# Kernel tuning notes

Measured on AMD Instinct MI355X. Metric: run time of the kernel, lower is better.

The kernel has to match this reference:

```python
import jax, jax.numpy as jnp
import numpy as np

N, D, K = 8192, 2048, 256
# amnesic weights at train iteration 0: _i = 2 < n1 = 20 -> l = 0
W1 = 0.5  # (_i - 1 - l) / _i
W2 = 0.5  # (1 + l) / _i


def setup_inputs() -> dict:
    key = jax.random.key(0)
    k1, k2 = jax.random.split(key)
    x = jax.random.normal(k1, (N, D), dtype=jnp.float32)
    V0 = 0.1 * jax.random.normal(k2, (D, K), dtype=jnp.float32)  # init eigen vectors
    return {"x": x, "V0": V0}


def reference(x, V0):
    # x: [N, D] input batch; V0: [D, K] unnormalized eigenvector estimates (_v)
    d0 = jnp.linalg.norm(V0, axis=0)  # per-column norms, as in init_eigen_vectors setter

    def step(r, inp):
        v, d = inp  # v: [D] current unnormalized component, d: scalar norm
        # CCIPCA update: v' = w1*v + w2 * r^T (r v) / d
        u = W1 * v + (W2 / d) * (r.T @ (r @ v))
        dn = jnp.linalg.norm(u)
        vn = u / dn
        # deflate residual: r <- r - (r vn) vn^T
        r = r - jnp.outer(r @ vn, vn)
        return r, vn

    _, vns = jax.lax.scan(step, x, (V0.T, d0))  # vns: [K, D] normalized components
    # project original input on updated components: x.mm(self.v)
    return x @ vns.T  # [N, K]
```

## Files before the change

### kernel.cpp

```cpp
#include <hip/hip_runtime.h>
#include <math.h>

#define NN 8192
#define DD 2048
#define KK 256
#define NB 256
#define RPB 8
#define NGRP 16
#define GSZ 16

__device__ __forceinline__ float blockReduceSum(float val, float* sdata) {
    for (int off = 32; off > 0; off >>= 1)
        val += __shfl_down(val, off, 64);
    int wid = threadIdx.x >> 6;
    int lane = threadIdx.x & 63;
    __syncthreads();
    if (lane == 0) sdata[wid] = val;
    __syncthreads();
    return sdata[0] + sdata[1] + sdata[2] + sdata[3];
}

__device__ __forceinline__ float agload(const float* p) {
    return __hip_atomic_load(p, __ATOMIC_RELAXED, __HIP_MEMORY_SCOPE_AGENT);
}
__device__ __forceinline__ void agstore(float* p, float v) {
    __hip_atomic_store(p, v, __ATOMIC_RELAXED, __HIP_MEMORY_SCOPE_AGENT);
}

__device__ __forceinline__ void gbar2(unsigned* bar, int b, unsigned* gen_local) {
    __syncthreads();
    if (threadIdx.x == 0) {
        unsigned g0 = *gen_local;
        int grp = b >> 4;
        unsigned* gcnt = bar + (size_t)grp * 64;
        unsigned* ggen = bar + 1024 + (size_t)grp * 64;
        unsigned* rcnt = bar + 2048;
        unsigned* rgen = bar + 2112;
        unsigned prev = __hip_atomic_fetch_add(gcnt, 1u, __ATOMIC_RELAXED, __HIP_MEMORY_SCOPE_AGENT);
        if (prev == GSZ - 1u) {
            unsigned prevr = __hip_atomic_fetch_add(rcnt, 1u, __ATOMIC_RELAXED, __HIP_MEMORY_SCOPE_AGENT);
            if (prevr == NGRP - 1u) {
                __hip_atomic_store(rcnt, 0u, __ATOMIC_RELAXED, __HIP_MEMORY_SCOPE_AGENT);
                asm volatile("s_waitcnt vmcnt(0)" ::: "memory");
                __hip_atomic_store(rgen, g0 + 1u, __ATOMIC_RELAXED, __HIP_MEMORY_SCOPE_AGENT);
            } else {
                while (__hip_atomic_load(rgen, __ATOMIC_RELAXED, __HIP_MEMORY_SCOPE_AGENT) == g0)
                    __builtin_amdgcn_s_sleep(1);
            }
            __hip_atomic_store(gcnt, 0u, __ATOMIC_RELAXED, __HIP_MEMORY_SCOPE_AGENT);
            asm volatile("s_waitcnt vmcnt(0)" ::: "memory");
            __hip_atomic_store(ggen, g0 + 1u, __ATOMIC_RELAXED, __HIP_MEMORY_SCOPE_AGENT);
        } else {
            while (__hip_atomic_load(ggen, __ATOMIC_RELAXED, __HIP_MEMORY_SCOPE_AGENT) == g0)
                __builtin_amdgcn_s_sleep(1);
        }
    }
    *gen_local += 1u;
    __syncthreads();
}

__global__ void ktranspose(const float* __restrict__ V0, float* __restrict__ V0T) {
    __shared__ float tile[32][33];
    int bx = blockIdx.x;
    int by = blockIdx.y;
    int tx = threadIdx.x % 32;
    int ty = threadIdx.x / 32;
    for (int r = ty; r < 32; r += 8)
        tile[r][tx] = V0[(size_t)(bx * 32 + r) * KK + by * 32 + tx];
    __syncthreads();
    for (int r = ty; r < 32; r += 8)
        V0T[(size_t)(by * 32 + r) * DD + bx * 32 + tx] = tile[tx][r];
}

__global__ void kd0(const float* __restrict__ V0T, float* __restrict__ d0) {
    __shared__ float sdata[4];
    int k = blockIdx.x;
    float acc = 0.f;
    for (int j = threadIdx.x; j < DD; j += 256) {
        float v = V0T[(size_t)k * DD + j];
        acc += v * v;
    }
    float s = blockReduceSum(acc, sdata);
    if (threadIdx.x == 0) d0[k] = sqrtf(s);
}

__global__ void ksyrk(const float* __restrict__ x, float* __restrict__ G) {
    __shared__ float As[32][68];
    __shared__ float Bs[32][68];
    int t = blockIdx.x;
    int bj = (int)((sqrtf(8.0f * (float)t + 1.0f) - 1.0f) * 0.5f);
    while ((bj + 1) * (bj + 2) / 2 <= t) ++bj;
    while (bj * (bj + 1) / 2 > t) --bj;
    int bi = t - bj * (bj + 1) / 2;
    int a0 = bi * 64, b0 = bj * 64;
    int tid = threadIdx.x;
    int al = tid % 64;
    int nl0 = tid / 64;
    int tr = tid / 16, tc = tid % 16;
    float acc[4][4] = {};
    for (int n0 = 0; n0 < NN; n0 += 32) {
        for (int pass = 0; pass < 8; ++pass) {
            int nl = nl0 + pass * 4;
            As[nl][al] = x[(size_t)(n0 + nl) * DD + a0 + al];
            Bs[nl][al] = x[(size_t)(n0 + nl) * DD + b0 + al];
        }
        __syncthreads();
        for (int kk2 = 0; kk2 < 32; ++kk2) {
            float4 a4 = *(const float4*)&As[kk2][tr * 4];
            float4 b4 = *(const float4*)&Bs[kk2][tc * 4];
            float a[4] = {a4.x, a4.y, a4.z, a4.w};
            float b[4] = {b4.x, b4.y, b4.z, b4.w};
            for (int i = 0; i < 4; ++i)
                for (int j = 0; j < 4; ++j)
                    acc[i][j] += a[i] * b[j];
        }
        __syncthreads();
    }
    for (int i = 0; i < 4; ++i) {
        float4 o = make_float4(acc[i][0], acc[i][1], acc[i][2], acc[i][3]);
        *(float4*)&G[(size_t)(a0 + tr * 4 + i) * DD + b0 + tc * 4] = o;
    }
    if (bi != bj) {
        for (int i = 0; i < 4; ++i)
            for (int j = 0; j < 4; ++j)
                G[(size_t)(b0 + tc * 4 + j) * DD + a0 + tr * 4 + i] = acc[i][j];
    }
}

__global__ void kmatvecG(const float* __restrict__ G, const float* __restrict__ v,
                         float* __restrict__ s) {
    __shared__ float vs[DD];
    int tid = threadIdx.x;
    for (int t2 = 0; t2 < 8; ++t2) vs[tid + t2 * 256] = v[tid + t2 * 256];
    __syncthreads();
    int wave = tid >> 6, lane = tid & 63;
    int row = blockIdx.x * 4 + wave;
    const float* Gr = G + (size_t)row * DD;
    float a = 0.f;
    for (int c = 0; c < 8; ++c) {
        int idx = lane * 4 + c * 256;
        float4 gq = *(const float4*)(Gr + idx);
        float4 vq = *(const float4*)(vs + idx);
        a += gq.x * vq.x + gq.y * vq.y + gq.z * vq.z + gq.w * vq.w;
    }
    for (int off = 32; off > 0; off >>= 1) a += __shfl_down(a, off, 64);
    if (lane == 0) s[row] = a;
}

__global__ void kstep1(const float* __restrict__ G, const float* __restrict__ V0T,
                       const float* __restrict__ d0, const float* __restrict__ s,
                       float* __restrict__ g, float* __restrict__ Vn, int k) {
    __shared__ float u[DD];
    __shared__ float sdata[4];
    __shared__ float sinv;
    int tid = threadIdx.x;
    const float* v = V0T + (size_t)k * DD;
    float cf = 0.5f / d0[k];
    float acc = 0.f;
    for (int t2 = 0; t2 < 8; ++t2) {
        int j = tid + t2 * 256;
        float uj = 0.5f * v[j] + cf * s[j];
        u[j] = uj;
        acc += uj * uj;
    }
    float n2 = blockReduceSum(acc, sdata);
    if (tid == 0) sinv = 1.0f / sqrtf(n2);
    __syncthreads();
    float inv = sinv;
    if (blockIdx.x == 0) {
        for (int t2 = 0; t2 < 8; ++t2) {
            int j = tid + t2 * 256;
            Vn[(size_t)k * DD + j] = u[j] * inv;
        }
    }
    int wave = tid >> 6, lane = tid & 63;
    int row = blockIdx.x * 4 + wave;
    const float* Gr = G + (size_t)row * DD;
    float a = 0.f;
    for (int c = 0; c < 8; ++c) {
        int idx = lane * 4 + c * 256;
        float4 gq = *(const float4*)(Gr + idx);
        float4 uq = *(const float4*)(u + idx);
        a += gq.x * uq.x + gq.y * uq.y + gq.z * uq.z + gq.w * uq.w;
    }
    for (int off = 32; off > 0; off >>= 1) a += __shfl_down(a, off, 64);
    if (lane == 0) g[row] = a * inv;
}

__global__ void kstep2(float* __restrict__ G, const float* __restrict__ V0T,
                       const float* __restrict__ Vn, const float* __restrict__ g,
                       float* __restrict__ s_next, int k, int knext) {
    __shared__ float vn_s[DD];
    __shared__ float h_s[DD];
    __shared__ float w_s[DD];
    __shared__ float sdata[4];
    int tid = threadIdx.x;
    float acc = 0.f;
    for (int t2 = 0; t2 < 8; ++t2) {
        int j = tid + t2 * 256;
        float vnj = Vn[(size_t)k * DD + j];
        float gj = g[j];
        vn_s[j] = vnj;
        h_s[j] = gj;
        w_s[j] = V0T[(size_t)knext * DD + j];
        acc += vnj * gj;
    }
    float c = blockReduceSum(acc, sdata);
    for (int t2 = 0; t2 < 8; ++t2) {
        int j = tid + t2 * 256;
        h_s[j] -= c * vn_s[j];
    }
    __syncthreads();
    int wave = tid >> 6, lane = tid & 63;
    int row = blockIdx.x * 4 + wave;
    float vni = vn_s[row], gi = g[row];
    float* Gr = G + (size_t)row * DD;
    float a = 0.f;
    for (int cc = 0; cc < 8; ++cc) {
        int idx = lane * 4 + cc * 256;
        float4 Gq = *(float4*)(Gr + idx);
        float4 hq = *(const float4*)(h_s + idx);
        float4 vq = *(const float4*)(vn_s + idx);
        float4 wq = *(const float4*)(w_s + idx);
        Gq.x = Gq.x - vni * hq.x - gi * vq.x;
        Gq.y = Gq.y - vni * hq.y - gi * vq.y;
        Gq.z = Gq.z - vni * hq.z - gi * vq.z;
        Gq.w = Gq.w - vni * hq.w - gi * vq.w;
        a += Gq.x * wq.x + Gq.y * wq.y + Gq.z * wq.z + Gq.w * wq.w;
        *(float4*)(Gr + idx) = Gq;
    }
    for (int off = 32; off > 0; off >>= 1) a += __shfl_down(a, off, 64);
    if (lane == 0) s_next[row] = a;
}

__global__ void __launch_bounds__(1024, 4) kloop2(
    float* __restrict__ G, const float* __restrict__ V0T,
    const float* __restrict__ d0, float* __restrict__ Vn,
    float* __restrict__ gbuf, float* __restrict__ wbuf,
    unsigned* bar) {
    __shared__ float vbuf[2][DD];
    __shared__ float gs[DD];
    __shared__ float vx[DD];
    __shared__ float redA[16], redB[16], redC[16];
    __shared__ float partg[16], partw[16];
    const int tid = threadIdx.x;
    const int b = blockIdx.x;
    const int wave = tid >> 6, lane = tid & 63;
    const int rowi = wave >> 1;
    const int half = wave & 1;
    const int row = b * RPB + rowi;
    float* Gr = G + (size_t)row * DD;
    unsigned gen = 0;

    vbuf[0][tid] = 0.f;
    vbuf[0][tid + 1024] = 0.f;
    vx[tid] = V0T[tid];
    vx[tid + 1024] = V0T[tid + 1024];
    __syncthreads();
    {
        float aw = 0.f;
        for (int c = 0; c < 4; ++c) {
            int idx = half * 1024 + lane * 4 + c * 256;
            float4 g4 = *(const float4*)(Gr + idx);
            float4 x4 = *(const float4*)(vx + idx);
            aw += g4.x * x4.x + g4.y * x4.y + g4.z * x4.z + g4.w * x4.w;
        }
        for (int off = 32; off > 0; off >>= 1) aw += __shfl_down(aw, off, 64);
        if (lane == 0) partw[wave] = aw;
    }
    __syncthreads();
    if (tid < RPB)
        agstore(&wbuf[b * RPB + tid], partw[2 * tid] + partw[2 * tid + 1]);
    gbar2(bar, b, &gen);

    for (int k = 0; k < KK; ++k) {
        const int p = k & 1;
        const float* vnp = vbuf[p];
        float* vnew = vbuf[p ^ 1];
        const float* gsrc = gbuf + (size_t)p * DD;
        const float* wsrc = wbuf + (size_t)p * DD;
        float* gdst = gbuf + (size_t)(p ^ 1) * DD;
        float* wdst = wbuf + (size_t)(p ^ 1) * DD;
        const float* vk = V0T + (size_t)k * DD;

        float vk0 = vk[tid], vk1 = vk[tid + 1024];
        float g0 = agload(&gsrc[tid]), g1 = agload(&gsrc[tid + 1024]);
        gs[tid] = g0;
        gs[tid + 1024] = g1;
        float vp0 = vnp[tid], vp1 = vnp[tid + 1024];
        float pc = vp0 * g0 + vp1 * g1;
        float pgv = g0 * vk0 + g1 * vk1;
        float pbv = vp0 * vk0 + vp1 * vk1;
        for (int off = 32; off > 0; off >>= 1) {
            pc += __shfl_down(pc, off, 64);
            pgv += __shfl_down(pgv, off, 64);
            pbv += __shfl_down(pbv, off, 64);
        }
        __syncthreads();
        if (lane == 0) { redA[wave] = pc; redB[wave] = pgv; redC[wave] = pbv; }
        __syncthreads();
        float c_s = 0.f, gv = 0.f, bv = 0.f;
        for (int i = 0; i < 16; ++i) { c_s += redA[i]; gv += redB[i]; bv += redC[i]; }
        float alpha = gv - c_s * bv;
        float beta = bv;

        float cf = 0.5f / d0[k];
        float w0 = agload(&wsrc[tid]), w1 = agload(&wsrc[tid + 1024]);
        float u0 = 0.5f * vk0 + cf * (w0 - alpha * vp0 - beta * g0);
        float u1 = 0.5f * vk1 + cf * (w1 - alpha * vp1 - beta * g1);
        float pn = u0 * u0 + u1 * u1;
        for (int off = 32; off > 0; off >>= 1) pn += __shfl_down(pn, off, 64);
        __syncthreads();
        if (lane == 0) redA[wave] = pn;
        __syncthreads();
        float n2 = 0.f;
        for (int i = 0; i < 16; ++i) n2 += redA[i];
        float inv = 1.0f / sqrtf(n2);

        if (b == 0) {
            Vn[(size_t)k * DD + tid] = u0 * inv;
            Vn[(size_t)k * DD + tid + 1024] = u1 * inv;
        }
        if (k == KK - 1) break;

        vnew[tid] = u0 * inv;
        vnew[tid + 1024] = u1 * inv;
        const float* vkn = V0T + (size_t)(k + 1) * DD;
        vx[tid] = vkn[tid];
        vx[tid + 1024] = vkn[tid + 1024];
        __syncthreads();

        {
            float a_r = vnp[row];
            float g_r = gs[row];
            float b_r = g_r - c_s * a_r;
            float ag = 0.f, aw = 0.f;
            for (int c = 0; c < 4; ++c) {
                int idx = half * 1024 + lane * 4 + c * 256;
                float4 G4 = *(float4*)(Gr + idx);
                float4 gq = *(const float4*)(gs + idx);
                float4 vq = *(const float4*)(vnp + idx);
                float4 nq = *(const float4*)(vnew + idx);
                float4 xq = *(const float4*)(vx + idx);
                G4.x -= a_r * gq.x + b_r * vq.x;
                G4.y -= a_r * gq.y + b_r * vq.y;
                G4.z -= a_r * gq.z + b_r * vq.z;
                G4.w -= a_r * gq.w + b_r * vq.w;
                ag += G4.x * nq.x + G4.y * nq.y + G4.z * nq.z + G4.w * nq.w;
                aw += G4.x * xq.x + G4.y * xq.y + G4.z * xq.z + G4.w * xq.w;
                *(float4*)(Gr + idx) = G4;
            }
            for (int off = 32; off > 0; off >>= 1) {
                ag += __shfl_down(ag, off, 64);
                aw += __shfl_down(aw, off, 64);
            }
            if (lane == 0) { partg[wave] = ag; partw[wave] = aw; }
        }
        __syncthreads();
        if (tid < RPB) {
            int r = b * RPB + tid;
            agstore(&gdst[r], partg[2 * tid] + partg[2 * tid + 1]);
            agstore(&wdst[r], partw[2 * tid] + partw[2 * tid + 1]);
        }
        gbar2(bar, b, &gen);
    }
}

__global__ void kout(const float* __restrict__ x, const float* __restrict__ Vn,
                     float* __restrict__ out) {
    __shared__ float As[32][68];
    __shared__ float Bs[32][68];
    int i0 = blockIdx.x * 64;
    int k0 = blockIdx.y * 64;
    int tid = threadIdx.x;
    int tr = tid / 16;
    int tc = tid % 16;
    float acc[4][4] = {};
    for (int j0 = 0; j0 < DD; j0 += 32) {
        int c = tid % 32;
        int r0 = tid / 32;
        for (int pass = 0; pass < 8; ++pass) {
            int rr = r0 + pass * 8;
            As[c][rr] = x[(size_t)(i0 + rr) * DD + j0 + c];
            Bs[c][rr] = Vn[(size_t)(k0 + rr) * DD + j0 + c];
        }
        __syncthreads();
        for (int kk = 0; kk < 32; ++kk) {
            float4 a4 = *(const float4*)&As[kk][tr * 4];
            float4 b4 = *(const float4*)&Bs[kk][tc * 4];
            float a[4] = {a4.x, a4.y, a4.z, a4.w};
            float b[4] = {b4.x, b4.y, b4.z, b4.w};
            for (int ar = 0; ar < 4; ++ar)
                for (int bc = 0; bc < 4; ++bc)
                    acc[ar][bc] += a[ar] * b[bc];
        }
        __syncthreads();
    }
    for (int ar = 0; ar < 4; ++ar) {
        float4 o = make_float4(acc[ar][0], acc[ar][1], acc[ar][2], acc[ar][3]);
        *(float4*)&out[(size_t)(i0 + tr * 4 + ar) * KK + k0 + tc * 4] = o;
    }
}

extern "C" void kernel_launch(void* const* d_in, const int* in_sizes, int n_in,
                              void* d_out, int out_size, void* d_ws, size_t ws_size,
                              hipStream_t stream) {
    const float* x  = (const float*)d_in[0];
    const float* V0 = (const float*)d_in[1];
    float* out = (float*)d_out;

    float* G    = (float*)d_ws;
    float* V0T  = G + (size_t)DD * DD;
    float* Vn   = V0T + (size_t)KK * DD;
    float* gbuf = Vn + (size_t)KK * DD;
    float* wbuf = gbuf + 2 * DD;
    float* d0   = wbuf + 2 * DD;
    unsigned* bar = (unsigned*)(d0 + KK);

    ktranspose<<<dim3(DD / 32, KK / 32), 256, 0, stream>>>(V0, V0T);
    kd0<<<KK, 256, 0, stream>>>(V0T, d0);
    ksyrk<<<528, 256, 0, stream>>>(x, G);

    hipMemsetAsync(bar, 0, 2176 * sizeof(unsigned), stream);
    hipMemsetAsync(gbuf, 0, DD * sizeof(float), stream);

    void* kargs[] = {(void*)&G, (void*)&V0T, (void*)&d0, (void*)&Vn,
                     (void*)&gbuf, (void*)&wbuf, (void*)&bar};
    hipError_t cerr = hipLaunchCooperativeKernel(kloop2, dim3(NB), dim3(1024),
                                                 kargs, 0, stream);
    if (cerr != hipSuccess) {
        float* g = gbuf;
        float* sbuf = wbuf;
        kmatvecG<<<512, 256, 0, stream>>>(G, V0T, sbuf);
        for (int k = 0; k < KK; ++k) {
            float* s_cur = sbuf + (k & 1) * DD;
            float* s_nxt = sbuf + ((k + 1) & 1) * DD;
            kstep1<<<512, 256, 0, stream>>>(G, V0T, d0, s_cur, g, Vn, k);
            if (k < KK - 1)
                kstep2<<<512, 256, 0, stream>>>(G, V0T, Vn, g, s_nxt, k, k + 1);
        }
    }

    kout<<<dim3(NN / 64, KK / 64), 256, 0, stream>>>(x, Vn, out);
}
```

Baseline: 2.872 ms.

## Defer Gram-matrix deflation updates into windowed blocked flushes

The persistent cooperative kernel used to rewrite the whole 2048x2048 Gram matrix G after every component. It now keeps a window of up to 8 pending rank-2 deflations, held as Vn and a new gwinG buffer, and applies them lazily. The matvec results are corrected with small dot-product reductions, and G is read once per step but written only at flush time. This cuts the global read-modify-write traffic on G, at the cost of extra reductions, syncs and global loads of the window vectors on each step.

```diff
diff --git a/kernel.cpp b/kernel.cpp
--- a/kernel.cpp
+++ b/kernel.cpp
@@ -8,6 +8,7 @@
 #define RPB 8
 #define NGRP 16
 #define GSZ 16
+#define TW 8
 
 __device__ __forceinline__ float blockReduceSum(float val, float* sdata) {
     for (int off = 32; off > 0; off >>= 1)
@@ -233,34 +234,41 @@
     if (lane == 0) s_next[row] = a;
 }
 
-__global__ void __launch_bounds__(1024, 4) kloop2(
+__global__ void __launch_bounds__(1024, 4) kloop3(
     float* __restrict__ G, const float* __restrict__ V0T,
-    const float* __restrict__ d0, float* __restrict__ Vn,
+    const float* __restrict__ d0v, float* __restrict__ Vn,
+    float* __restrict__ gwinG,
     float* __restrict__ gbuf, float* __restrict__ wbuf,
     unsigned* bar) {
-    __shared__ float vbuf[2][DD];
-    __shared__ float gs[DD];
+    __shared__ float vnew[DD];
     __shared__ float vx[DD];
-    __shared__ float redA[16], redB[16], redC[16];
+    __shared__ float stv[DD];
+    __shared__ float stg[DD];
+    __shared__ float redC[18][16];
+    __shared__ float redS[18];
+    __shared__ float redN[16];
     __shared__ float partg[16], partw[16];
+    __shared__ float cwin[TW];
+
     const int tid = threadIdx.x;
     const int b = blockIdx.x;
     const int wave = tid >> 6, lane = tid & 63;
     const int rowi = wave >> 1;
     const int half = wave & 1;
     const int row = b * RPB + rowi;
+    const int d0i = tid, d1i = tid + 1024;
+    const int ib = half * 1024 + lane * 4;
     float* Gr = G + (size_t)row * DD;
     unsigned gen = 0;
 
-    vbuf[0][tid] = 0.f;
-    vbuf[0][tid + 1024] = 0.f;
-    vx[tid] = V0T[tid];
-    vx[tid + 1024] = V0T[tid + 1024];
+    vx[d0i] = V0T[d0i];
+    vx[d1i] = V0T[d1i];
     __syncthreads();
     {
         float aw = 0.f;
+        #pragma unroll
         for (int c = 0; c < 4; ++c) {
-            int idx = half * 1024 + lane * 4 + c * 256;
+            int idx = ib + c * 256;
             float4 g4 = *(const float4*)(Gr + idx);
             float4 x4 = *(const float4*)(vx + idx);
             aw += g4.x * x4.x + g4.y * x4.y + g4.z * x4.z + g4.w * x4.w;
@@ -273,88 +281,227 @@
         agstore(&wbuf[b * RPB + tid], partw[2 * tid] + partw[2 * tid + 1]);
     gbar2(bar, b, &gen);
 
+    int base = 0;
     for (int k = 0; k < KK; ++k) {
         const int p = k & 1;
-        const float* vnp = vbuf[p];
-        float* vnew = vbuf[p ^ 1];
         const float* gsrc = gbuf + (size_t)p * DD;
         const float* wsrc = wbuf + (size_t)p * DD;
         float* gdst = gbuf + (size_t)(p ^ 1) * DD;
         float* wdst = wbuf + (size_t)(p ^ 1) * DD;
         const float* vk = V0T + (size_t)k * DD;
 
-        float vk0 = vk[tid], vk1 = vk[tid + 1024];
-        float g0 = agload(&gsrc[tid]), g1 = agload(&gsrc[tid + 1024]);
-        gs[tid] = g0;
-        gs[tid + 1024] = g1;
-        float vp0 = vnp[tid], vp1 = vnp[tid + 1024];
-        float pc = vp0 * g0 + vp1 * g1;
-        float pgv = g0 * vk0 + g1 * vk1;
-        float pbv = vp0 * vk0 + vp1 * vk1;
-        for (int off = 32; off > 0; off >>= 1) {
-            pc += __shfl_down(pc, off, 64);
-            pgv += __shfl_down(pgv, off, 64);
-            pbv += __shfl_down(pbv, off, 64);
-        }
-        __syncthreads();
-        if (lane == 0) { redA[wave] = pc; redB[wave] = pgv; redC[wave] = pbv; }
-        __syncthreads();
-        float c_s = 0.f, gv = 0.f, bv = 0.f;
-        for (int i = 0; i < 16; ++i) { c_s += redA[i]; gv += redB[i]; bv += redC[i]; }
-        float alpha = gv - c_s * bv;
-        float beta = bv;
-
-        float cf = 0.5f / d0[k];
-        float w0 = agload(&wsrc[tid]), w1 = agload(&wsrc[tid + 1024]);
-        float u0 = 0.5f * vk0 + cf * (w0 - alpha * vp0 - beta * g0);
-        float u1 = 0.5f * vk1 + cf * (w1 - alpha * vp1 - beta * g1);
+        float gh0 = agload(&gsrc[d0i]), gh1 = agload(&gsrc[d1i]);
+        float wh0 = agload(&wsrc[d0i]), wh1 = agload(&wsrc[d1i]);
+        float vk0 = vk[d0i], vk1 = vk[d1i];
+
+        const int pend = k - 1;
+        const int mc1 = (k > 0) ? (pend - base) : 0;
+        const int mc2 = (k > 0) ? (k - base) : 0;
+
+        float wv0[7], wv1[7], wg0[7], wg1[7];
+        #pragma unroll
+        for (int jj = 0; jj < 7; ++jj) {
+            if (jj < mc1) {
+                const float* vj = Vn + (size_t)(base + jj) * DD;
+                const float* gj = gwinG + (size_t)(base + jj) * DD;
+                wv0[jj] = vj[d0i]; wv1[jj] = vj[d1i];
+                wg0[jj] = gj[d0i]; wg1[jj] = gj[d1i];
+            }
+        }
+
+        float gc0 = gh0, gc1 = gh1;
+        float vp0 = 0.f, vp1 = 0.f;
+        if (k > 0) { vp0 = vnew[d0i]; vp1 = vnew[d1i]; }
+        if (mc1 > 0) {
+            #pragma unroll
+            for (int jj = 0; jj < 7; ++jj) {
+                if (jj < mc1) {
+                    float pa = wg0[jj] * vp0 + wg1[jj] * vp1;
+                    float pb = wv0[jj] * vp0 + wv1[jj] * vp1;
+                    for (int off = 32; off > 0; off >>= 1) {
+                        pa += __shfl_down(pa, off, 64);
+                        pb += __shfl_down(pb, off, 64);
+                    }
+                    if (lane == 0) { redC[2 * jj][wave] = pa; redC[2 * jj + 1][wave] = pb; }
+                }
+            }
+            __syncthreads();
+            if (wave == 0 && lane < 2 * mc1) {
+                float s = 0.f;
+                for (int w = 0; w < 16; ++w) s += redC[lane][w];
+                redS[lane] = s;
+            }
+            __syncthreads();
+            #pragma unroll
+            for (int jj = 0; jj < 7; ++jj) {
+                if (jj < mc1) {
+                    float A_ = redS[2 * jj], B_ = redS[2 * jj + 1];
+                    float cj = cwin[jj];
+                    float hA = A_ - cj * B_;
+                    gc0 -= wv0[jj] * hA + wg0[jj] * B_;
+                    gc1 -= wv1[jj] * hA + wg1[jj] * B_;
+                }
+            }
+        }
+
+        float c_s = 0.f;
+        float s0 = wh0, s1 = wh1;
+        if (k > 0) {
+            float pc = vp0 * gc0 + vp1 * gc1;
+            for (int off = 32; off > 0; off >>= 1) pc += __shfl_down(pc, off, 64);
+            if (lane == 0) redC[0][wave] = pc;
+            #pragma unroll
+            for (int jj = 0; jj < 7; ++jj) {
+                if (jj < mc1) {
+                    float pP = wg0[jj] * vk0 + wg1[jj] * vk1;
+                    float pQ = wv0[jj] * vk0 + wv1[jj] * vk1;
+                    for (int off = 32; off > 0; off >>= 1) {
+                        pP += __shfl_down(pP, off, 64);
+                        pQ += __shfl_down(pQ, off, 64);
+                    }
+                    if (lane == 0) { redC[1 + 2 * jj][wave] = pP; redC[2 + 2 * jj][wave] = pQ; }
+                }
+            }
+            {
+                float pP = gc0 * vk0 + gc1 * vk1;
+                float pQ = vp0 * vk0 + vp1 * vk1;
+                for (int off = 32; off > 0; off >>= 1) {
+                    pP += __shfl_down(pP, off, 64);
+                    pQ += __shfl_down(pQ, off, 64);
+                }
+                if (lane == 0) { redC[1 + 2 * mc1][wave] = pP; redC[2 + 2 * mc1][wave] = pQ; }
+            }
+            __syncthreads();
+            int nv = 1 + 2 * mc2;
+            if (wave == 0 && lane < nv) {
+                float s = 0.f;
+                for (int w = 0; w < 16; ++w) s += redC[lane][w];
+                redS[lane] = s;
+            }
+            __syncthreads();
+            c_s = redS[0];
+            if (tid == 0) cwin[pend & (TW - 1)] = c_s;
+            #pragma unroll
+            for (int jj = 0; jj < 7; ++jj) {
+                if (jj < mc1) {
+                    float P_ = redS[1 + 2 * jj], Q_ = redS[2 + 2 * jj];
+                    float cj = cwin[jj];
+                    float hP = P_ - cj * Q_;
+                    s0 -= wv0[jj] * hP + wg0[jj] * Q_;
+                    s1 -= wv1[jj] * hP + wg1[jj] * Q_;
+                }
+            }
+            {
+                float P_ = redS[1 + 2 * mc1], Q_ = redS[2 + 2 * mc1];
+                float hP = P_ - c_s * Q_;
+                s0 -= vp0 * hP + gc0 * Q_;
+                s1 -= vp1 * hP + gc1 * Q_;
+            }
+        }
+
+        float cf = 0.5f / d0v[k];
+        float u0 = 0.5f * vk0 + cf * s0;
+        float u1 = 0.5f * vk1 + cf * s1;
         float pn = u0 * u0 + u1 * u1;
         for (int off = 32; off > 0; off >>= 1) pn += __shfl_down(pn, off, 64);
-        __syncthreads();
-        if (lane == 0) redA[wave] = pn;
-        __syncthreads();
+        if (lane == 0) redN[wave] = pn;
+        __syncthreads();
+
+        const bool flush = (k < KK - 1) && (mc2 == TW);
+        if (flush) {
+            stv[d0i] = vp0; stv[d1i] = vp1;
+            stg[d0i] = gc0; stg[d1i] = gc1;
+        }
         float n2 = 0.f;
-        for (int i = 0; i < 16; ++i) n2 += redA[i];
+        #pragma unroll
+        for (int w = 0; w < 16; ++w) n2 += redN[w];
         float inv = 1.0f / sqrtf(n2);
-
+        float o0 = u0 * inv, o1 = u1 * inv;
+        vnew[d0i] = o0;
+        vnew[d1i] = o1;
         if (b == 0) {
-            Vn[(size_t)k * DD + tid] = u0 * inv;
-            Vn[(size_t)k * DD + tid + 1024] = u1 * inv;
+            agstore(&Vn[(size_t)k * DD + d0i], o0);
+            agstore(&Vn[(size_t)k * DD + d1i], o1);
+            if (k > 0) {
+                agstore(&gwinG[(size_t)pend * DD + d0i], gc0);
+                agstore(&gwinG[(size_t)pend * DD + d1i], gc1);
+            }
         }
         if (k == KK - 1) break;
-
-        vnew[tid] = u0 * inv;
-        vnew[tid + 1024] = u1 * inv;
-        const float* vkn = V0T + (size_t)(k + 1) * DD;
-        vx[tid] = vkn[tid];
-        vx[tid + 1024] = vkn[tid + 1024];
-        __syncthreads();
+        vx[d0i] = V0T[(size_t)(k + 1) * DD + d0i];
+        vx[d1i] = V0T[(size_t)(k + 1) * DD + d1i];
+        __syncthreads();
+
+        float4 Gq0 = *(float4*)(Gr + ib);
+        float4 Gq1 = *(float4*)(Gr + ib + 256);
+        float4 Gq2 = *(float4*)(Gr + ib + 512);
+        float4 Gq3 = *(float4*)(Gr + ib + 768);
+
+        if (flush) {
+            {
+                float av = stv[row];
+                float agr = stg[row];
+                float bv = agr - c_s * av;
+                #pragma unroll
+                for (int c = 0; c < 4; ++c) {
+                    int idx = ib + c * 256;
+                    float4 sg = *(const float4*)(stg + idx);
+                    float4 sv = *(const float4*)(stv + idx);
+                    float4* Gq = (c == 0) ? &Gq0 : (c == 1) ? &Gq1 : (c == 2) ? &Gq2 : &Gq3;
+                    Gq->x -= av * sg.x + bv * sv.x;
+                    Gq->y -= av * sg.y + bv * sv.y;
+                    Gq->z -= av * sg.z + bv * sv.z;
+                    Gq->w -= av * sg.w + bv * sv.w;
+                }
+            }
+            #pragma unroll
+            for (int jj = 0; jj < TW - 1; ++jj) {
+                __syncthreads();
+                const float* vj = Vn + (size_t)(base + jj) * DD;
+                const float* gj = gwinG + (size_t)(base + jj) * DD;
+                stv[d0i] = vj[d0i]; stv[d1i] = vj[d1i];
+                stg[d0i] = gj[d0i]; stg[d1i] = gj[d1i];
+                __syncthreads();
+                float av = stv[row];
+                float agr = stg[row];
+                float bv = agr - cwin[jj] * av;
+                #pragma unroll
+                for (int c = 0; c < 4; ++c) {
+                    int idx = ib + c * 256;
+                    float4 sg = *(const float4*)(stg + idx);
+                    float4 sv = *(const float4*)(stv + idx);
+                    float4* Gq = (c == 0) ? &Gq0 : (c == 1) ? &Gq1 : (c == 2) ? &Gq2 : &Gq3;
+                    Gq->x -= av * sg.x + bv * sv.x;
+                    Gq->y -= av * sg.y + bv * sv.y;
+                    Gq->z -= av * sg.z + bv * sv.z;
+                    Gq->w -= av * sg.w + bv * sv.w;
+                }
+            }
+            base = k;
+        }
 
         {
-            float a_r = vnp[row];
-            float g_r = gs[row];
-            float b_r = g_r - c_s * a_r;
-            float ag = 0.f, aw = 0.f;
+            float agd = 0.f, awd = 0.f;
+            #pragma unroll
             for (int c = 0; c < 4; ++c) {
-                int idx = half * 1024 + lane * 4 + c * 256;
-                float4 G4 = *(float4*)(Gr + idx);
-                float4 gq = *(const float4*)(gs + idx);
-                float4 vq = *(const float4*)(vnp + idx);
+                int idx = ib + c * 256;
                 float4 nq = *(const float4*)(vnew + idx);
                 float4 xq = *(const float4*)(vx + idx);
-                G4.x -= a_r * gq.x + b_r * vq.x;
-                G4.y -= a_r * gq.y + b_r * vq.y;
-                G4.z -= a_r * gq.z + b_r * vq.z;
-                G4.w -= a_r * gq.w + b_r * vq.w;
-                ag += G4.x * nq.x + G4.y * nq.y + G4.z * nq.z + G4.w * nq.w;
-                aw += G4.x * xq.x + G4.y * xq.y + G4.z * xq.z + G4.w * xq.w;
-                *(float4*)(Gr + idx) = G4;
+                float4 Gq = (c == 0) ? Gq0 : (c == 1) ? Gq1 : (c == 2) ? Gq2 : Gq3;
+                agd += Gq.x * nq.x + Gq.y * nq.y + Gq.z * nq.z + Gq.w * nq.w;
+                awd += Gq.x * xq.x + Gq.y * xq.y + Gq.z * xq.z + Gq.w * xq.w;
+            }
+            if (flush) {
+                *(float4*)(Gr + ib) = Gq0;
+                *(float4*)(Gr + ib + 256) = Gq1;
+                *(float4*)(Gr + ib + 512) = Gq2;
+                *(float4*)(Gr + ib + 768) = Gq3;
             }
             for (int off = 32; off > 0; off >>= 1) {
-                ag += __shfl_down(ag, off, 64);
-                aw += __shfl_down(aw, off, 64);
-            }
-            if (lane == 0) { partg[wave] = ag; partw[wave] = aw; }
+                agd += __shfl_down(agd, off, 64);
+                awd += __shfl_down(awd, off, 64);
+            }
+            if (lane == 0) { partg[wave] = agd; partw[wave] = awd; }
         }
         __syncthreads();
         if (tid < RPB) {
@@ -409,12 +556,13 @@
     const float* V0 = (const float*)d_in[1];
     float* out = (float*)d_out;
 
-    float* G    = (float*)d_ws;
-    float* V0T  = G + (size_t)DD * DD;
-    float* Vn   = V0T + (size_t)KK * DD;
-    float* gbuf = Vn + (size_t)KK * DD;
-    float* wbuf = gbuf + 2 * DD;
-    float* d0   = wbuf + 2 * DD;
+    float* G     = (float*)d_ws;
+    float* V0T   = G + (size_t)DD * DD;
+    float* Vn    = V0T + (size_t)KK * DD;
+    float* gwinG = Vn + (size_t)KK * DD;
+    float* gbuf  = gwinG + (size_t)KK * DD;
+    float* wbuf  = gbuf + 2 * DD;
+    float* d0    = wbuf + 2 * DD;
     unsigned* bar = (unsigned*)(d0 + KK);
 
     ktranspose<<<dim3(DD / 32, KK / 32), 256, 0, stream>>>(V0, V0T);
@@ -422,11 +570,10 @@
     ksyrk<<<528, 256, 0, stream>>>(x, G);
 
     hipMemsetAsync(bar, 0, 2176 * sizeof(unsigned), stream);
-    hipMemsetAsync(gbuf, 0, DD * sizeof(float), stream);
 
     void* kargs[] = {(void*)&G, (void*)&V0T, (void*)&d0, (void*)&Vn,
-                     (void*)&gbuf, (void*)&wbuf, (void*)&bar};
-    hipError_t cerr = hipLaunchCooperativeKernel(kloop2, dim3(NB), dim3(1024),
+                     (void*)&gwinG, (void*)&gbuf, (void*)&wbuf, (void*)&bar};
+    hipError_t cerr = hipLaunchCooperativeKernel(kloop3, dim3(NB), dim3(1024),
                                                  kargs, 0, stream);
     if (cerr != hipSuccess) {
         float* g = gbuf;
```

Result: slower. 4.039 ms (+40.6%).

## Keep G rows in registers and precompute step scalars via global atomics

Applied to the files above, without the earlier changes.

Each block now keeps its slice of the deflated Gram matrix in registers across all 256 iterations instead of reloading and storing it from global memory every step. The per-step block reductions (dot products and the norm of u) are replaced by eight scalar accumulators. All blocks add into these with atomics during the previous step, and the norm is reconstructed algebraically, which removes several __syncthreads/reduction rounds per iteration. Vn output is written distributed across blocks. The risk is higher register pressure and possible cancellation error in the expanded norm formula.

```diff
diff --git a/kernel.cpp b/kernel.cpp
--- a/kernel.cpp
+++ b/kernel.cpp
@@ -233,44 +233,61 @@
     if (lane == 0) s_next[row] = a;
 }
 
-__global__ void __launch_bounds__(1024, 4) kloop2(
+__global__ void __launch_bounds__(1024, 4) kloop4(
     float* __restrict__ G, const float* __restrict__ V0T,
-    const float* __restrict__ d0, float* __restrict__ Vn,
+    const float* __restrict__ d0v, float* __restrict__ Vn,
     float* __restrict__ gbuf, float* __restrict__ wbuf,
-    unsigned* bar) {
+    float* __restrict__ acc, unsigned* bar) {
     __shared__ float vbuf[2][DD];
     __shared__ float gs[DD];
     __shared__ float vx[DD];
-    __shared__ float redA[16], redB[16], redC[16];
     __shared__ float partg[16], partw[16];
+
     const int tid = threadIdx.x;
     const int b = blockIdx.x;
     const int wave = tid >> 6, lane = tid & 63;
     const int rowi = wave >> 1;
     const int half = wave & 1;
     const int row = b * RPB + rowi;
-    float* Gr = G + (size_t)row * DD;
+    const int d0i = tid, d1i = tid + 1024;
+    const int ib = half * 1024 + lane * 4;
+    const float* Gr = G + (size_t)row * DD;
     unsigned gen = 0;
 
-    vbuf[0][tid] = 0.f;
-    vbuf[0][tid + 1024] = 0.f;
-    vx[tid] = V0T[tid];
-    vx[tid + 1024] = V0T[tid + 1024];
+    float4 Gq[4];
+    #pragma unroll
+    for (int c = 0; c < 4; ++c) Gq[c] = *(const float4*)(Gr + ib + c * 256);
+
+    vbuf[0][d0i] = 0.f;
+    vbuf[0][d1i] = 0.f;
+    vx[d0i] = V0T[d0i];
+    vx[d1i] = V0T[d1i];
     __syncthreads();
     {
         float aw = 0.f;
+        #pragma unroll
         for (int c = 0; c < 4; ++c) {
-            int idx = half * 1024 + lane * 4 + c * 256;
-            float4 g4 = *(const float4*)(Gr + idx);
-            float4 x4 = *(const float4*)(vx + idx);
-            aw += g4.x * x4.x + g4.y * x4.y + g4.z * x4.z + g4.w * x4.w;
+            float4 xq = *(const float4*)(vx + ib + c * 256);
+            aw += Gq[c].x * xq.x + Gq[c].y * xq.y + Gq[c].z * xq.z + Gq[c].w * xq.w;
         }
         for (int off = 32; off > 0; off >>= 1) aw += __shfl_down(aw, off, 64);
         if (lane == 0) partw[wave] = aw;
     }
     __syncthreads();
-    if (tid < RPB)
-        agstore(&wbuf[b * RPB + tid], partw[2 * tid] + partw[2 * tid + 1]);
+    if (tid < RPB) {
+        int rg = b * RPB + tid;
+        agstore(&wbuf[rg], partw[2 * tid] + partw[2 * tid + 1]);
+    }
+    if (tid == 0) {
+        float a4 = 0.f, a7 = 0.f;
+        for (int r = 0; r < RPB; ++r) {
+            float wr = partw[2 * r] + partw[2 * r + 1];
+            a4 += wr * wr;
+            a7 += wr * vx[b * RPB + r];
+        }
+        atomicAdd(&acc[3], a4);
+        atomicAdd(&acc[6], a7);
+    }
     gbar2(bar, b, &gen);
 
     for (int k = 0; k < KK; ++k) {
@@ -282,73 +299,62 @@
         float* gdst = gbuf + (size_t)(p ^ 1) * DD;
         float* wdst = wbuf + (size_t)(p ^ 1) * DD;
         const float* vk = V0T + (size_t)k * DD;
-
-        float vk0 = vk[tid], vk1 = vk[tid + 1024];
-        float g0 = agload(&gsrc[tid]), g1 = agload(&gsrc[tid + 1024]);
-        gs[tid] = g0;
-        gs[tid + 1024] = g1;
-        float vp0 = vnp[tid], vp1 = vnp[tid + 1024];
-        float pc = vp0 * g0 + vp1 * g1;
-        float pgv = g0 * vk0 + g1 * vk1;
-        float pbv = vp0 * vk0 + vp1 * vk1;
-        for (int off = 32; off > 0; off >>= 1) {
-            pc += __shfl_down(pc, off, 64);
-            pgv += __shfl_down(pgv, off, 64);
-            pbv += __shfl_down(pbv, off, 64);
-        }
-        __syncthreads();
-        if (lane == 0) { redA[wave] = pc; redB[wave] = pgv; redC[wave] = pbv; }
-        __syncthreads();
-        float c_s = 0.f, gv = 0.f, bv = 0.f;
-        for (int i = 0; i < 16; ++i) { c_s += redA[i]; gv += redB[i]; bv += redC[i]; }
-        float alpha = gv - c_s * bv;
-        float beta = bv;
-
-        float cf = 0.5f / d0[k];
-        float w0 = agload(&wsrc[tid]), w1 = agload(&wsrc[tid + 1024]);
+        const float* as = acc + (size_t)k * 8;
+
+        float A1 = agload(&as[0]), A2 = agload(&as[1]), A3 = agload(&as[2]);
+        float A4 = agload(&as[3]), A5 = agload(&as[4]), A6 = agload(&as[5]);
+        float A7 = agload(&as[6]), A8 = agload(&as[7]);
+        float d0k = d0v[k];
+        float cf = 0.5f / d0k;
+        float c_s = A1;
+        float alpha = A2 - A1 * A3;
+        float beta = A3;
+        float ss = A4 + alpha * alpha + beta * beta * A8
+                 - 2.f * alpha * A6 - 2.f * beta * A5 + 2.f * alpha * beta * A1;
+        float vks = A7 - alpha * A3 - beta * A2;
+        float n2 = 0.25f * d0k * d0k + cf * vks + cf * cf * ss;
+        float inv = 1.0f / sqrtf(n2);
+
+        float g0 = agload(&gsrc[d0i]), g1 = agload(&gsrc[d1i]);
+        float w0 = agload(&wsrc[d0i]), w1 = agload(&wsrc[d1i]);
+        float vk0 = vk[d0i], vk1 = vk[d1i];
+        float vp0 = vnp[d0i], vp1 = vnp[d1i];
+        gs[d0i] = g0;
+        gs[d1i] = g1;
         float u0 = 0.5f * vk0 + cf * (w0 - alpha * vp0 - beta * g0);
         float u1 = 0.5f * vk1 + cf * (w1 - alpha * vp1 - beta * g1);
-        float pn = u0 * u0 + u1 * u1;
-        for (int off = 32; off > 0; off >>= 1) pn += __shfl_down(pn, off, 64);
-        __syncthreads();
-        if (lane == 0) redA[wave] = pn;
-        __syncthreads();
-        float n2 = 0.f;
-        for (int i = 0; i < 16; ++i) n2 += redA[i];
-        float inv = 1.0f / sqrtf(n2);
-
-        if (b == 0) {
-            Vn[(size_t)k * DD + tid] = u0 * inv;
-            Vn[(size_t)k * DD + tid + 1024] = u1 * inv;
+        vnew[d0i] = u0 * inv;
+        vnew[d1i] = u1 * inv;
+        if (k < KK - 1) {
+            vx[d0i] = V0T[(size_t)(k + 1) * DD + d0i];
+            vx[d1i] = V0T[(size_t)(k + 1) * DD + d1i];
+        }
+        __syncthreads();
+
+        if (tid < RPB) {
+            int rg = b * RPB + tid;
+            agstore(&Vn[(size_t)k * DD + rg], vnew[rg]);
         }
         if (k == KK - 1) break;
-
-        vnew[tid] = u0 * inv;
-        vnew[tid + 1024] = u1 * inv;
-        const float* vkn = V0T + (size_t)(k + 1) * DD;
-        vx[tid] = vkn[tid];
-        vx[tid + 1024] = vkn[tid + 1024];
-        __syncthreads();
 
         {
             float a_r = vnp[row];
             float g_r = gs[row];
             float b_r = g_r - c_s * a_r;
             float ag = 0.f, aw = 0.f;
+            #pragma unroll
             for (int c = 0; c < 4; ++c) {
-                int idx = half * 1024 + lane * 4 + c * 256;
-                float4 G4 = *(float4*)(Gr + idx);
+                int idx = ib + c * 256;
                 float4 gq = *(const float4*)(gs + idx);
                 float4 vq = *(const float4*)(vnp + idx);
                 float4 nq = *(const float4*)(vnew + idx);
                 float4 xq = *(const float4*)(vx + idx);
-                G4.x -= a_r * gq.x + b_r * vq.x;
-                G4.y -= a_r * gq.y + b_r * vq.y;
-                G4.z -= a_r * gq.z + b_r * vq.z;
-                G4.w -= a_r * gq.w + b_r * vq.w;
-                ag += G4.x * nq.x + G4.y * nq.y + G4.z * nq.z + G4.w * nq.w;
-                aw += G4.x * xq.x + G4.y * xq.y + G4.z * xq.z + G4.w * xq.w;
-                *(float4*)(Gr + idx) = G4;
+                Gq[c].x -= a_r * gq.x + b_r * vq.x;
+                Gq[c].y -= a_r * gq.y + b_r * vq.y;
+                Gq[c].z -= a_r * gq.z + b_r * vq.z;
+                Gq[c].w -= a_r * gq.w + b_r * vq.w;
+                ag += Gq[c].x * nq.x + Gq[c].y * nq.y + Gq[c].z * nq.z + Gq[c].w * nq.w;
+                aw += Gq[c].x * xq.x + Gq[c].y * xq.y + Gq[c].z * xq.z + Gq[c].w * xq.w;
             }
             for (int off = 32; off > 0; off >>= 1) {
                 ag += __shfl_down(ag, off, 64);
@@ -358,9 +364,32 @@
         }
         __syncthreads();
         if (tid < RPB) {
-            int r = b * RPB + tid;
-            agstore(&gdst[r], partg[2 * tid] + partg[2 * tid + 1]);
-            agstore(&wdst[r], partw[2 * tid] + partw[2 * tid + 1]);
+            int rg = b * RPB + tid;
+            agstore(&gdst[rg], partg[2 * tid] + partg[2 * tid + 1]);
+            agstore(&wdst[rg], partw[2 * tid] + partw[2 * tid + 1]);
+        }
+        if (tid < 8) {
+            float sacc = 0.f;
+            for (int r = 0; r < RPB; ++r) {
+                int rg = b * RPB + r;
+                float gr = partg[2 * r] + partg[2 * r + 1];
+                float wr = partw[2 * r] + partw[2 * r + 1];
+                float vnr = vnew[rg];
+                float vxr = vx[rg];
+                float t;
+                switch (tid) {
+                    case 0: t = vnr * gr; break;
+                    case 1: t = gr * vxr; break;
+                    case 2: t = vnr * vxr; break;
+                    case 3: t = wr * wr; break;
+                    case 4: t = wr * gr; break;
+                    case 5: t = wr * vnr; break;
+                    case 6: t = wr * vxr; break;
+                    default: t = gr * gr; break;
+                }
+                sacc += t;
+            }
+            atomicAdd(&acc[(size_t)(k + 1) * 8 + tid], sacc);
         }
         gbar2(bar, b, &gen);
     }
@@ -415,7 +444,8 @@
     float* gbuf = Vn + (size_t)KK * DD;
     float* wbuf = gbuf + 2 * DD;
     float* d0   = wbuf + 2 * DD;
-    unsigned* bar = (unsigned*)(d0 + KK);
+    float* acc  = d0 + KK;
+    unsigned* bar = (unsigned*)(acc + (size_t)KK * 8);
 
     ktranspose<<<dim3(DD / 32, KK / 32), 256, 0, stream>>>(V0, V0T);
     kd0<<<KK, 256, 0, stream>>>(V0T, d0);
@@ -423,10 +453,11 @@
 
     hipMemsetAsync(bar, 0, 2176 * sizeof(unsigned), stream);
     hipMemsetAsync(gbuf, 0, DD * sizeof(float), stream);
+    hipMemsetAsync(acc, 0, (size_t)KK * 8 * sizeof(float), stream);
 
     void* kargs[] = {(void*)&G, (void*)&V0T, (void*)&d0, (void*)&Vn,
-                     (void*)&gbuf, (void*)&wbuf, (void*)&bar};
-    hipError_t cerr = hipLaunchCooperativeKernel(kloop2, dim3(NB), dim3(1024),
+                     (void*)&gbuf, (void*)&wbuf, (void*)&acc, (void*)&bar};
+    hipError_t cerr = hipLaunchCooperativeKernel(kloop4, dim3(NB), dim3(1024),
                                                  kargs, 0, stream);
     if (cerr != hipSuccess) {
         float* g = gbuf;
```

Result: slower. 3.471 ms (+20.8%).
